# Kernel tuning notes

Measured on AMD Instinct MI355X. Metric: run time of the kernel, lower is better.

Reference implementation:

```python
import jax, jax.numpy as jnp
import numpy as np

EMBED = 1024
HEADS = 16
HEAD_DIM = EMBED // HEADS


def _rope(t):
    # t: (B, S, H, D) -> rotary embedding applied over last dim (GPT-NeoX rotate-half)
    B, S, H, D = t.shape
    half = D // 2
    inv_freq = 1.0 / (10000.0 ** (jnp.arange(0, half, dtype=jnp.float32) / half))
    freqs = jnp.arange(S, dtype=jnp.float32)[:, None] * inv_freq[None, :]  # (S, half)
    cos = jnp.cos(freqs)[None, :, None, :]
    sin = jnp.sin(freqs)[None, :, None, :]
    t1, t2 = t[..., :half], t[..., half:]
    return jnp.concatenate([t1 * cos - t2 * sin, t2 * cos + t1 * sin], axis=-1)


def setup_inputs() -> dict:
    key = jax.random.key(0)
    k1, k2, k3 = jax.random.split(key, 3)
    B, S = 2, 2048
    x = jax.random.normal(k1, (B, S, EMBED), dtype=jnp.float32)
    attn_mask = jnp.ones((B, S), dtype=bool)
    w_qkv = jax.random.normal(k2, (EMBED, 3 * EMBED), dtype=jnp.float32) * (1.0 / np.sqrt(EMBED))
    w_out = jax.random.normal(k3, (EMBED, EMBED), dtype=jnp.float32) * (1.0 / np.sqrt(EMBED))
    return {"x": x, "attn_mask": attn_mask, "w_qkv": w_qkv, "w_out": w_out, "is_causal": 1}


def reference(x, attn_mask, w_qkv, w_out, is_causal):
    B, S, E = x.shape
    qkv = x @ w_qkv                                   # (B, S, 3E)
    q, k, v = jnp.split(qkv, 3, axis=-1)
    q = q.reshape(B, S, HEADS, HEAD_DIM)
    k = k.reshape(B, S, HEADS, HEAD_DIM)
    v = v.reshape(B, S, HEADS, HEAD_DIM)
    q = _rope(q)
    k = _rope(k)
    scale = 1.0 / np.sqrt(HEAD_DIM)
    scores = jnp.einsum('bqhd,bkhd->bhqk', q, k) * scale  # (B, H, S, S)
    neg = jnp.asarray(-1e30, dtype=scores.dtype)
    if is_causal:
        causal = jnp.tril(jnp.ones((S, S), dtype=bool))
        scores = jnp.where(causal[None, None], scores, neg)
    else:
        scores = jnp.where(attn_mask[:, None, None, :], scores, neg)
    attn = jax.nn.softmax(scores, axis=-1)
    y = jnp.einsum('bhqk,bkhd->bqhd', attn, v).reshape(B, S, E)
    return y @ w_out
```

## Files before the change

### kernel.cpp

```cpp
#include <hip/hip_runtime.h>
#include <hip/hip_bf16.h>
#include <stdint.h>

typedef float v4f __attribute__((ext_vector_type(4)));
typedef short v8s __attribute__((ext_vector_type(8)));

#define LOG2E 1.44269504088896f
#define QSCALE (0.125f * LOG2E)
#define SOFTMAX_OFF 16.0f

__device__ __forceinline__ unsigned short f2bf(float f) {
    unsigned int u = __float_as_uint(f);
    u += 0x7fffu + ((u >> 16) & 1u);
    return (unsigned short)(u >> 16);
}

#define LDS_FENCE() __builtin_amdgcn_fence(__ATOMIC_ACQ_REL, "workgroup")

__device__ __forceinline__ void gload_lds16(const unsigned short* g, unsigned short* s) {
    __builtin_amdgcn_global_load_lds(
        (const __attribute__((address_space(1))) unsigned int*)g,
        (__attribute__((address_space(3))) unsigned int*)s, 16, 0, 0);
}

#define BAR()      asm volatile("s_barrier" ::: "memory")
#define VMWAIT(N)  asm volatile("s_waitcnt vmcnt(" #N ")" ::: "memory")
#define LGKM0()    do { asm volatile("s_waitcnt lgkmcnt(0)" ::: "memory"); \
                        __builtin_amdgcn_sched_barrier(0); } while (0)

#define PIPE_BARRIER_KEEP4()                                   \
    do {                                                       \
        asm volatile("s_waitcnt vmcnt(4)" ::: "memory");       \
        __builtin_amdgcn_s_barrier();                          \
        asm volatile("" ::: "memory");                         \
    } while (0)
#define PIPE_BARRIER_DRAIN()                                   \
    do {                                                       \
        asm volatile("s_waitcnt vmcnt(0)" ::: "memory");       \
        __builtin_amdgcn_s_barrier();                          \
        asm volatile("" ::: "memory");                         \
    } while (0)

__global__ void k_prep(const float* __restrict__ x,
                       const float* __restrict__ w_qkv,
                       const float* __restrict__ w_out,
                       unsigned short* __restrict__ xb,
                       unsigned short* __restrict__ wqkvT,
                       unsigned short* __restrict__ woutT,
                       float2* __restrict__ rope) {
    __shared__ unsigned short tile[64][65];
    int id = blockIdx.x, t = threadIdx.x;
    if (id < 1024) {
        int base = id * 256 + t;
#pragma unroll
        for (int k = 0; k < 4; ++k) {
            int i = base + k * 262144;
            float4 v = ((const float4*)x)[i];
            ushort4 o;
            o.x = f2bf(v.x); o.y = f2bf(v.y); o.z = f2bf(v.z); o.w = f2bf(v.w);
            ((ushort4*)xb)[i] = o;
        }
        return;
    }
    id -= 1024;
    if (id < 256) {
        int idx = id * 256 + t;
        int s = idx >> 5, d = idx & 31;
        float inv = __expf(-(float)d * 0.28782313662425572f);
        float sn, cs;
        sincosf((float)s * inv, &sn, &cs);
        rope[idx] = make_float2(cs, sn);
        return;
    }
    id -= 256;
    const float* src; unsigned short* dst; int N, kb, nb;
    if (id < 768) { src = w_qkv; dst = wqkvT; N = 3072; nb = (id % 48) * 64; kb = (id / 48) * 64; }
    else { id -= 768; src = w_out; dst = woutT; N = 1024; nb = (id % 16) * 64; kb = (id / 16) * 64; }
    const int K = 1024;
    for (int i = 0; i < 16; ++i) {
        int e = t + i * 256;
        int n_l = e & 63, k_l = e >> 6;
        tile[n_l][k_l] = f2bf(src[(size_t)(kb + k_l) * N + nb + n_l]);
    }
    __syncthreads();
    for (int i = 0; i < 16; ++i) {
        int e = t + i * 256;
        int k_l = e & 63, n_l = e >> 6;
        dst[(size_t)(nb + n_l) * K + kb + k_l] = tile[n_l][k_l];
    }
}

__global__ __launch_bounds__(512, 2) void k_gemm_qkv(
    const unsigned short* __restrict__ A,
    const unsigned short* __restrict__ Bt,
    const float2* __restrict__ rope,
    unsigned short* __restrict__ Qg,
    unsigned short* __restrict__ Kg,
    unsigned short* __restrict__ Vt) {
    const int K = 1024;
    __shared__ __align__(16) union {
        struct { unsigned short Ab[2][256 * 64], Bb[2][256 * 64]; } g;
        unsigned short vt[4][64][264];
    } sm;
    const int t = threadIdx.x;
    const int w = t >> 6, l = t & 63, quad = l >> 4, ln = l & 15;
    const int wr = w >> 2, wc = w & 3;
    const int mb = blockIdx.y * 256, nb = blockIdx.x * 256;
    const int lxr = l >> 3;
    const int swz = ((l & 7) ^ lxr) * 8;

    v4f acc[8][4];
#pragma unroll
    for (int i = 0; i < 8; ++i)
#pragma unroll
        for (int j = 0; j < 4; ++j) acc[i][j] = (v4f){0.f, 0.f, 0.f, 0.f};

    auto stageHT = [&](const unsigned short* src, int grow, int k0, unsigned short* lds) {
#pragma unroll
        for (int c = 0; c < 2; ++c) {
            int r0 = w * 16 + c * 8;
            gload_lds16(src + (size_t)(grow + r0 + lxr) * K + k0 + swz, lds + r0 * 64);
        }
    };
    auto frag = [&](const unsigned short* base, int row, int g16) -> v8s {
        return *(const v8s*)&base[row * 64 + ((g16 ^ (row & 7)) << 3)];
    };

    v8s aF[4][2], bF0[2][2], bF1[2][2];
    auto readA = [&](const unsigned short* Ap, int ih) {
#pragma unroll
        for (int ii = 0; ii < 4; ++ii) {
            int row = wr * 128 + (ih * 4 + ii) * 16 + ln;
#pragma unroll
            for (int kh = 0; kh < 2; ++kh) aF[ii][kh] = frag(Ap, row, kh * 4 + quad);
        }
    };
    auto readB = [&](const unsigned short* Bp, int jh, v8s (&bF)[2][2]) {
#pragma unroll
        for (int jj = 0; jj < 2; ++jj) {
            int row = wc * 64 + (jh * 2 + jj) * 16 + ln;
#pragma unroll
            for (int kh = 0; kh < 2; ++kh) bF[jj][kh] = frag(Bp, row, kh * 4 + quad);
        }
    };
    auto mfma16 = [&](v8s (&bF)[2][2], int ih, int jh) {
        __builtin_amdgcn_s_setprio(1);
#pragma unroll
        for (int ii = 0; ii < 4; ++ii)
#pragma unroll
            for (int jj = 0; jj < 2; ++jj) {
                v4f* ac = &acc[ih * 4 + ii][jh * 2 + jj];
                *ac = __builtin_amdgcn_mfma_f32_16x16x32_bf16(aF[ii][0], bF[jj][0], *ac, 0, 0, 0);
                *ac = __builtin_amdgcn_mfma_f32_16x16x32_bf16(aF[ii][1], bF[jj][1], *ac, 0, 0, 0);
            }
        __builtin_amdgcn_s_setprio(0);
        __builtin_amdgcn_sched_barrier(0);
    };

    const unsigned short* Ap0 = &sm.g.Ab[0][0];
    const unsigned short* Ap1 = &sm.g.Ab[1][0];
    const unsigned short* Bp0 = &sm.g.Bb[0][0];
    const unsigned short* Bp1 = &sm.g.Bb[1][0];

    stageHT(A,  mb,       0,  &sm.g.Ab[0][0]);
    stageHT(A,  mb + 128, 0,  &sm.g.Ab[0][128 * 64]);
    stageHT(Bt, nb,       0,  &sm.g.Bb[0][0]);
    stageHT(Bt, nb + 128, 0,  &sm.g.Bb[0][128 * 64]);
    stageHT(Bt, nb,       64, &sm.g.Bb[1][0]);
    stageHT(Bt, nb + 128, 64, &sm.g.Bb[1][128 * 64]);
    VMWAIT(4);
    BAR();

    for (int it = 0; it < 8; ++it) {
        const int c1k = (2 * it + 1) * 64, n0k = (2 * it + 2) * 64, n1k = (2 * it + 3) * 64;
        const bool pre = it < 7;
        readA(Ap0, 0); readB(Bp0, 0, bF0);
        stageHT(A, mb, c1k, &sm.g.Ab[1][0]);
        BAR(); LGKM0();
        mfma16(bF0, 0, 0);
        BAR();
        readB(Bp0, 1, bF1);
        stageHT(A, mb + 128, c1k, &sm.g.Ab[1][128 * 64]);
        BAR(); LGKM0();
        mfma16(bF1, 0, 1);
        BAR();
        readA(Ap0, 1);
        if (pre) stageHT(Bt, nb, n0k, &sm.g.Bb[0][0]);
        BAR(); LGKM0();
        mfma16(bF0, 1, 0);
        BAR();
        if (pre) stageHT(Bt, nb + 128, n0k, &sm.g.Bb[0][128 * 64]);
        BAR();
        mfma16(bF1, 1, 1);
        if (pre) VMWAIT(4); else VMWAIT(0);
        BAR();
        readA(Ap1, 0); readB(Bp1, 0, bF0);
        if (pre) stageHT(A, mb, n0k, &sm.g.Ab[0][0]);
        BAR(); LGKM0();
        mfma16(bF0, 0, 0);
        BAR();
        readB(Bp1, 1, bF1);
        if (pre) stageHT(A, mb + 128, n0k, &sm.g.Ab[0][128 * 64]);
        BAR(); LGKM0();
        mfma16(bF1, 0, 1);
        BAR();
        readA(Ap1, 1);
        if (pre) stageHT(Bt, nb, n1k, &sm.g.Bb[1][0]);
        BAR(); LGKM0();
        mfma16(bF0, 1, 0);
        BAR();
        if (pre) stageHT(Bt, nb + 128, n1k, &sm.g.Bb[1][128 * 64]);
        BAR();
        mfma16(bF1, 1, 1);
        if (pre) VMWAIT(4);
        BAR();
    }

    if (nb >= 2048) {
        __syncthreads();
#pragma unroll
        for (int i = 0; i < 8; ++i)
#pragma unroll
            for (int j = 0; j < 4; ++j) {
                int d = j * 16 + ln;
                int s0 = wr * 128 + i * 16 + quad * 4;
                ushort4 pk;
                pk.x = f2bf(acc[i][j][0]); pk.y = f2bf(acc[i][j][1]);
                pk.z = f2bf(acc[i][j][2]); pk.w = f2bf(acc[i][j][3]);
                *(ushort4*)&sm.vt[wc][d][s0] = pk;
            }
        __syncthreads();
        const int hbase = (nb & 1023) >> 6;
        const int b = mb >> 11, sbase = mb & 2047;
#pragma unroll
        for (int i = 0; i < 16; ++i) {
            int c = t + i * 512;
            int h2 = c >> 11, dd = (c >> 5) & 63, off = (c & 31) * 8;
            v8s val = *(const v8s*)&sm.vt[h2][dd][off];
            *(v8s*)(Vt + ((size_t)((b * 16 + hbase + h2) * 64 + dd) * 2048 + sbase + off)) = val;
        }
        return;
    }

    const int nbw = nb + wc * 64;
    const int region = nbw >> 10;
    const int h = (nbw & 1023) >> 6;
    unsigned short* dst = region == 0 ? Qg : Kg;
    const float scale = region == 0 ? QSCALE : 1.0f;
#pragma unroll
    for (int jj = 0; jj < 2; ++jj) {
        const float2* rp = rope + jj * 16 + ln;
#pragma unroll
        for (int i = 0; i < 8; ++i)
#pragma unroll
            for (int r = 0; r < 4; ++r) {
                int row = mb + wr * 128 + i * 16 + quad * 4 + r;
                int s = row & 2047, b = row >> 11;
                float2 cs = rp[s * 32];
                float t1 = acc[i][jj][r], t2 = acc[i][jj + 2][r];
                size_t base = ((size_t)(b * 16 + h) * 2048 + s) * 64;
                dst[base + jj * 16 + ln]      = f2bf((t1 * cs.x - t2 * cs.y) * scale);
                dst[base + jj * 16 + ln + 32] = f2bf((t2 * cs.x + t1 * cs.y) * scale);
            }
    }
}

__global__ __launch_bounds__(256) void k_gemm_out(
    const unsigned short* __restrict__ A,
    const unsigned short* __restrict__ Bt,
    float* __restrict__ C) {
    const int K = 1024, N = 1024;
    __shared__ __align__(16) unsigned short Ab[3][4096];
    __shared__ __align__(16) unsigned short Bb[3][4096];
    const int t = threadIdx.x;
    const int w = t >> 6, l = t & 63, quad = l >> 4, ln = l & 15;
    const int wm = (w >> 1) * 64, wn = (w & 1) * 64;
    const int mb = blockIdx.y * 128, nb = blockIdx.x * 128;

    v4f acc[4][4];
#pragma unroll
    for (int i = 0; i < 4; ++i)
#pragma unroll
        for (int j = 0; j < 4; ++j) acc[i][j] = (v4f){0.f, 0.f, 0.f, 0.f};

    auto stage = [&](int buf, int k0) {
#pragma unroll
        for (int u = 0; u < 2; ++u) {
            int e = t + u * 256;
            gload_lds16(A + (size_t)(mb + (e >> 2)) * K + k0 + (e & 3) * 8,
                        &Ab[buf][(w * 64 + u * 256) * 8]);
            gload_lds16(Bt + (size_t)(nb + (e >> 2)) * K + k0 + (e & 3) * 8,
                        &Bb[buf][(w * 64 + u * 256) * 8]);
        }
    };

    stage(0, 0);
    stage(1, 32);
    int cur = 0, nxt = 2;
    for (int itk = 0; itk < 32; ++itk) {
        if (itk < 31) PIPE_BARRIER_KEEP4();
        else          PIPE_BARRIER_DRAIN();
        if (itk + 2 < 32) {
            stage(nxt, (itk + 2) * 32);
            nxt = nxt == 2 ? 0 : nxt + 1;
        }
        v8s af[4], bfr[4];
#pragma unroll
        for (int i = 0; i < 4; ++i)
            af[i] = *(const v8s*)&Ab[cur][(wm + i * 16 + ln) * 32 + quad * 8];
#pragma unroll
        for (int j = 0; j < 4; ++j)
            bfr[j] = *(const v8s*)&Bb[cur][(wn + j * 16 + ln) * 32 + quad * 8];
#pragma unroll
        for (int i = 0; i < 4; ++i)
#pragma unroll
            for (int j = 0; j < 4; ++j)
                acc[i][j] = __builtin_amdgcn_mfma_f32_16x16x32_bf16(
                    af[i], bfr[j], acc[i][j], 0, 0, 0);
        cur = cur == 2 ? 0 : cur + 1;
    }

#pragma unroll
    for (int i = 0; i < 4; ++i) {
        int r0 = mb + wm + i * 16 + quad * 4;
#pragma unroll
        for (int j = 0; j < 4; ++j) {
            int c0 = nb + wn + j * 16 + ln;
#pragma unroll
            for (int r = 0; r < 4; ++r)
                C[(size_t)(r0 + r) * N + c0] = acc[i][j][r];
        }
    }
}

__global__ __launch_bounds__(256) void k_flash(
    const unsigned short* __restrict__ Qg,
    const unsigned short* __restrict__ Kg,
    const unsigned short* __restrict__ Vt,
    unsigned short* __restrict__ Og) {
    __shared__ __align__(16) unsigned short Kb[2][64 * 64];
    __shared__ __align__(16) unsigned short Vb[2][64 * 64];
    __shared__ __align__(16) unsigned short P[4][16][72];

    const int id = blockIdx.x;
    const int xcd = id & 7, slot = id >> 3;
    const int bh = xcd * 4 + (slot & 3);
    const int qt = 31 - (slot >> 2);
    const int qbase = qt * 64;
    const int nit = qt + 1;

    const int t = threadIdx.x, w = t >> 6, l = t & 63, quad = l >> 4, ln = l & 15;
    const int b = bh >> 4, h = bh & 15;

    const unsigned short* Qp = Qg + (size_t)bh * 2048 * 64;
    const unsigned short* Kp = Kg + (size_t)bh * 2048 * 64;
    const unsigned short* Vp = Vt + (size_t)bh * 64 * 2048;

    unsigned kst[2], vst[2];
    int cchunk = l & 7, rloc = l >> 3;
#pragma unroll
    for (int j = 0; j < 2; ++j) {
        int c = w + j * 4;
        int rr = c * 8 + rloc;
        int g = (cchunk + rr) & 7;
        kst[j] = (unsigned)(rr * 64 + g * 8);
        vst[j] = (unsigned)(rr * 2048 + g * 8);
    }
    const int c0 = ((quad - ln) & 7) * 8;
    const int c1 = ((quad + 4 - ln) & 7) * 8;
    const v8s ones = {0x3F80, 0x3F80, 0x3F80, 0x3F80, 0x3F80, 0x3F80, 0x3F80, 0x3F80};

    const int qrow = qbase + w * 16 + ln;
    v8s qf0 = *(const v8s*)(Qp + (size_t)qrow * 64 + quad * 8);
    v8s qf1 = *(const v8s*)(Qp + (size_t)qrow * 64 + quad * 8 + 32);

    v4f oacc[5];
#pragma unroll
    for (int dt = 0; dt < 5; ++dt) oacc[dt] = (v4f){0.f, 0.f, 0.f, 0.f};

    auto stage = [&](int buf, int kvb) {
        const unsigned short* kg = Kp + (size_t)kvb * 64;
        const unsigned short* vg = Vp + kvb;
#pragma unroll
        for (int j = 0; j < 2; ++j) {
            int c = w + j * 4;
            gload_lds16(kg + kst[j], &Kb[buf][c * 512]);
            gload_lds16(vg + vst[j], &Vb[buf][c * 512]);
        }
    };

    auto compute = [&](int buf, int it) {
        v4f sc[4];
#pragma unroll
        for (int kt = 0; kt < 4; ++kt) {
            int row = kt * 16 + ln;
            v8s k0 = *(const v8s*)&Kb[buf][row * 64 + c0];
            v8s k1 = *(const v8s*)&Kb[buf][row * 64 + c1];
            sc[kt] = (v4f){0.f, 0.f, 0.f, 0.f};
            sc[kt] = __builtin_amdgcn_mfma_f32_16x16x32_bf16(qf0, k0, sc[kt], 0, 0, 0);
            sc[kt] = __builtin_amdgcn_mfma_f32_16x16x32_bf16(qf1, k1, sc[kt], 0, 0, 0);
        }
        if (it == qt) {
            int q0 = qbase + w * 16 + quad * 4;
#pragma unroll
            for (int kt = 0; kt < 4; ++kt) {
                int kv = qbase + kt * 16 + ln;
#pragma unroll
                for (int r = 0; r < 4; ++r)
                    if (kv > q0 + r) sc[kt][r] = -1e30f;
            }
        }
#pragma unroll
        for (int kt = 0; kt < 4; ++kt)
#pragma unroll
            for (int r = 0; r < 4; ++r)
                sc[kt][r] = exp2f(sc[kt][r] - SOFTMAX_OFF);

#pragma unroll
        for (int kt = 0; kt < 4; ++kt) {
            union { __hip_bfloat162 hh; unsigned int u; } p01, p23;
            p01.hh = __float22bfloat162_rn(make_float2(sc[kt][0], sc[kt][1]));
            p23.hh = __float22bfloat162_rn(make_float2(sc[kt][2], sc[kt][3]));
            P[w][quad * 4 + 0][kt * 16 + ln] = (unsigned short)p01.u;
            P[w][quad * 4 + 1][kt * 16 + ln] = (unsigned short)(p01.u >> 16);
            P[w][quad * 4 + 2][kt * 16 + ln] = (unsigned short)p23.u;
            P[w][quad * 4 + 3][kt * 16 + ln] = (unsigned short)(p23.u >> 16);
        }
        LDS_FENCE();
        v8s pf0 = *(const v8s*)&P[w][ln][quad * 8];
        v8s pf1 = *(const v8s*)&P[w][ln][quad * 8 + 32];
        LDS_FENCE();
        __builtin_amdgcn_s_setprio(1);
#pragma unroll
        for (int dt = 0; dt < 4; ++dt) {
            int row = dt * 16 + ln;
            v8s v0 = *(const v8s*)&Vb[buf][row * 64 + c0];
            v8s v1 = *(const v8s*)&Vb[buf][row * 64 + c1];
            oacc[dt] = __builtin_amdgcn_mfma_f32_16x16x32_bf16(pf0, v0, oacc[dt], 0, 0, 0);
            oacc[dt] = __builtin_amdgcn_mfma_f32_16x16x32_bf16(pf1, v1, oacc[dt], 0, 0, 0);
        }
        oacc[4] = __builtin_amdgcn_mfma_f32_16x16x32_bf16(pf0, ones, oacc[4], 0, 0, 0);
        oacc[4] = __builtin_amdgcn_mfma_f32_16x16x32_bf16(pf1, ones, oacc[4], 0, 0, 0);
        __builtin_amdgcn_s_setprio(0);
    };

    stage(0, 0);
    for (int it = 0;;) {
        const int buf = it & 1;
        stage(buf ^ 1, (it + 1) * 64);
        VMWAIT(4);
        BAR();
        compute(buf, it);
        if (++it >= nit) break;
        BAR();
    }

    float rden[4];
#pragma unroll
    for (int r = 0; r < 4; ++r) rden[r] = 1.f / oacc[4][r];
#pragma unroll
    for (int dt = 0; dt < 4; ++dt)
#pragma unroll
        for (int r = 0; r < 4; ++r) {
            int s = qbase + w * 16 + quad * 4 + r;
            Og[(size_t)(b * 2048 + s) * 1024 + h * 64 + dt * 16 + ln] =
                f2bf(oacc[dt][r] * rden[r]);
        }
}

extern "C" void kernel_launch(void* const* d_in, const int* in_sizes, int n_in,
                              void* d_out, int out_size, void* d_ws, size_t ws_size,
                              hipStream_t stream) {
    const float* x     = (const float*)d_in[0];
    const float* w_qkv = (const float*)d_in[2];
    const float* w_out = (const float*)d_in[3];
    char* ws = (char*)d_ws;

    unsigned short* xb    = (unsigned short*)(ws);
    unsigned short* wqkvT = (unsigned short*)(ws + (size_t)(8 << 20));
    unsigned short* woutT = (unsigned short*)(ws + (size_t)(14 << 20));
    unsigned short* Qg    = (unsigned short*)(ws + (size_t)(16 << 20));
    unsigned short* Kg    = (unsigned short*)(ws + (size_t)(24 << 20));
    unsigned short* Vt    = (unsigned short*)(ws + (size_t)(32 << 20));
    unsigned short* Og    = (unsigned short*)(ws + (size_t)(40 << 20));
    float2*         rope  = (float2*)(ws + (size_t)(48 << 20));

    k_prep<<<2304, 256, 0, stream>>>(x, w_qkv, w_out, xb, wqkvT, woutT, rope);
    k_gemm_qkv<<<dim3(12, 16), 512, 0, stream>>>(xb, wqkvT, rope, Qg, Kg, Vt);
    k_flash<<<1024, 256, 0, stream>>>(Qg, Kg, Vt, Og);
    k_gemm_out<<<dim3(8, 32), 256, 0, stream>>>(Og, woutT, (float*)d_out);
}
```

Baseline: 199.0 us.

## Pair causal query tiles per flash block and vectorize QK epilogue stores via LDS

The flash attention kernel now processes two query tiles per block, a short one and its complementary long one, so every block does a balanced amount of causal work and reuses each staged K/V tile for both query tiles. The grid is halved accordingly. The QKV GEMM epilogue writes rotated Q/K values into a padded per-wave LDS buffer and then emits 16-byte coalesced global stores instead of scattered 2-byte stores. Costs are higher register pressure from two accumulator sets and a larger shared-memory union.

```diff
diff --git a/kernel.cpp b/kernel.cpp
--- a/kernel.cpp
+++ b/kernel.cpp
@@ -101,6 +101,7 @@
     __shared__ __align__(16) union {
         struct { unsigned short Ab[2][256 * 64], Bb[2][256 * 64]; } g;
         unsigned short vt[4][64][264];
+        unsigned short qk[8][128][66];
     } sm;
     const int t = threadIdx.x;
     const int w = t >> 6, l = t & 63, quad = l >> 4, ln = l & 15;
@@ -247,6 +248,7 @@
     const int h = (nbw & 1023) >> 6;
     unsigned short* dst = region == 0 ? Qg : Kg;
     const float scale = region == 0 ? QSCALE : 1.0f;
+    unsigned short* qkw = &sm.qk[w][0][0];
 #pragma unroll
     for (int jj = 0; jj < 2; ++jj) {
         const float2* rp = rope + jj * 16 + ln;
@@ -254,14 +256,24 @@
         for (int i = 0; i < 8; ++i)
 #pragma unroll
             for (int r = 0; r < 4; ++r) {
-                int row = mb + wr * 128 + i * 16 + quad * 4 + r;
-                int s = row & 2047, b = row >> 11;
+                int lr = i * 16 + quad * 4 + r;
+                int s = (mb + wr * 128 + lr) & 2047;
                 float2 cs = rp[s * 32];
                 float t1 = acc[i][jj][r], t2 = acc[i][jj + 2][r];
-                size_t base = ((size_t)(b * 16 + h) * 2048 + s) * 64;
-                dst[base + jj * 16 + ln]      = f2bf((t1 * cs.x - t2 * cs.y) * scale);
-                dst[base + jj * 16 + ln + 32] = f2bf((t2 * cs.x + t1 * cs.y) * scale);
+                qkw[lr * 66 + jj * 16 + ln]      = f2bf((t1 * cs.x - t2 * cs.y) * scale);
+                qkw[lr * 66 + jj * 16 + ln + 32] = f2bf((t2 * cs.x + t1 * cs.y) * scale);
             }
+    }
+    LDS_FENCE();
+    const int row0 = mb + wr * 128;
+    const int bb = row0 >> 11, s0 = row0 & 2047;
+    unsigned short* gbase = dst + ((size_t)(bb * 16 + h) * 2048 + s0) * 64;
+#pragma unroll
+    for (int itn = 0; itn < 16; ++itn) {
+        int c = itn * 64 + l;
+        int lr = c >> 3, off = (c & 7) * 8;
+        v8s val = *(const v8s*)&qkw[lr * 66 + off];
+        *(v8s*)(gbase + (size_t)lr * 64 + off) = val;
     }
 }
 
@@ -345,9 +357,9 @@
     const int id = blockIdx.x;
     const int xcd = id & 7, slot = id >> 3;
     const int bh = xcd * 4 + (slot & 3);
-    const int qt = 31 - (slot >> 2);
-    const int qbase = qt * 64;
-    const int nit = qt + 1;
+    const int pair = slot >> 2;
+    const int qtA = pair;
+    const int qtB = 31 - pair;
 
     const int t = threadIdx.x, w = t >> 6, l = t & 63, quad = l >> 4, ln = l & 15;
     const int b = bh >> 4, h = bh & 15;
@@ -370,13 +382,19 @@
     const int c1 = ((quad + 4 - ln) & 7) * 8;
     const v8s ones = {0x3F80, 0x3F80, 0x3F80, 0x3F80, 0x3F80, 0x3F80, 0x3F80, 0x3F80};
 
-    const int qrow = qbase + w * 16 + ln;
-    v8s qf0 = *(const v8s*)(Qp + (size_t)qrow * 64 + quad * 8);
-    v8s qf1 = *(const v8s*)(Qp + (size_t)qrow * 64 + quad * 8 + 32);
-
-    v4f oacc[5];
-#pragma unroll
-    for (int dt = 0; dt < 5; ++dt) oacc[dt] = (v4f){0.f, 0.f, 0.f, 0.f};
+    const int qrA = qtA * 64 + w * 16 + ln;
+    const int qrB = qtB * 64 + w * 16 + ln;
+    v8s qfA0 = *(const v8s*)(Qp + (size_t)qrA * 64 + quad * 8);
+    v8s qfA1 = *(const v8s*)(Qp + (size_t)qrA * 64 + quad * 8 + 32);
+    v8s qfB0 = *(const v8s*)(Qp + (size_t)qrB * 64 + quad * 8);
+    v8s qfB1 = *(const v8s*)(Qp + (size_t)qrB * 64 + quad * 8 + 32);
+
+    v4f oaccA[5], oaccB[5];
+#pragma unroll
+    for (int dt = 0; dt < 5; ++dt) {
+        oaccA[dt] = (v4f){0.f, 0.f, 0.f, 0.f};
+        oaccB[dt] = (v4f){0.f, 0.f, 0.f, 0.f};
+    }
 
     auto stage = [&](int buf, int kvb) {
         const unsigned short* kg = Kp + (size_t)kvb * 64;
@@ -389,7 +407,7 @@
         }
     };
 
-    auto compute = [&](int buf, int it) {
+    auto computeT = [&](int buf, int it, int qt, v8s qf0, v8s qf1, v4f* oacc) {
         v4f sc[4];
 #pragma unroll
         for (int kt = 0; kt < 4; ++kt) {
@@ -401,10 +419,10 @@
             sc[kt] = __builtin_amdgcn_mfma_f32_16x16x32_bf16(qf1, k1, sc[kt], 0, 0, 0);
         }
         if (it == qt) {
-            int q0 = qbase + w * 16 + quad * 4;
+            int q0 = qt * 64 + w * 16 + quad * 4;
 #pragma unroll
             for (int kt = 0; kt < 4; ++kt) {
-                int kv = qbase + kt * 16 + ln;
+                int kv = qt * 64 + kt * 16 + ln;
 #pragma unroll
                 for (int r = 0; r < 4; ++r)
                     if (kv > q0 + r) sc[kt][r] = -1e30f;
@@ -447,25 +465,31 @@
     stage(0, 0);
     for (int it = 0;;) {
         const int buf = it & 1;
-        stage(buf ^ 1, (it + 1) * 64);
-        VMWAIT(4);
-        BAR();
-        compute(buf, it);
-        if (++it >= nit) break;
-        BAR();
-    }
-
-    float rden[4];
-#pragma unroll
-    for (int r = 0; r < 4; ++r) rden[r] = 1.f / oacc[4][r];
-#pragma unroll
-    for (int dt = 0; dt < 4; ++dt)
-#pragma unroll
-        for (int r = 0; r < 4; ++r) {
-            int s = qbase + w * 16 + quad * 4 + r;
-            Og[(size_t)(b * 2048 + s) * 1024 + h * 64 + dt * 16 + ln] =
-                f2bf(oacc[dt][r] * rden[r]);
-        }
+        if (it < qtB) { stage(buf ^ 1, (it + 1) * 64); VMWAIT(4); }
+        else          { VMWAIT(0); }
+        BAR();
+        if (it <= qtA) computeT(buf, it, qtA, qfA0, qfA1, oaccA);
+        computeT(buf, it, qtB, qfB0, qfB1, oaccB);
+        if (++it > qtB) break;
+        BAR();
+    }
+
+#pragma unroll
+    for (int tile = 0; tile < 2; ++tile) {
+        const v4f* oacc = tile == 0 ? oaccA : oaccB;
+        const int qbase = (tile == 0 ? qtA : qtB) * 64;
+        float rden[4];
+#pragma unroll
+        for (int r = 0; r < 4; ++r) rden[r] = 1.f / oacc[4][r];
+#pragma unroll
+        for (int dt = 0; dt < 4; ++dt)
+#pragma unroll
+            for (int r = 0; r < 4; ++r) {
+                int s = qbase + w * 16 + quad * 4 + r;
+                Og[(size_t)(b * 2048 + s) * 1024 + h * 64 + dt * 16 + ln] =
+                    f2bf(oacc[dt][r] * rden[r]);
+            }
+    }
 }
 
 extern "C" void kernel_launch(void* const* d_in, const int* in_sizes, int n_in,
@@ -487,6 +511,6 @@
 
     k_prep<<<2304, 256, 0, stream>>>(x, w_qkv, w_out, xb, wqkvT, woutT, rope);
     k_gemm_qkv<<<dim3(12, 16), 512, 0, stream>>>(xb, wqkvT, rope, Qg, Kg, Vt);
-    k_flash<<<1024, 256, 0, stream>>>(Qg, Kg, Vt, Og);
+    k_flash<<<512, 256, 0, stream>>>(Qg, Kg, Vt, Og);
     k_gemm_out<<<dim3(8, 32), 256, 0, stream>>>(Og, woutT, (float*)d_out);
 }
```

New measurement: 193.6 us. -2.7%, faster.

## Stage QKV epilogue through LDS and reuse K buffer for P in flash

Applied to the files above, without the earlier changes.

The QKV GEMM epilogue now writes the rotary-embedded Q/K values into a padded per-wave LDS tile and then copies them to global memory with coalesced 16-byte stores, replacing scattered 2-byte global stores. The flash kernel drops its separate P buffer and writes the probabilities into the already-consumed K buffer with an XOR swizzle, adding a barrier first so other waves are done with K. Together with a launch bound of 4 blocks per CU, this is meant to cut LDS use and raise occupancy. The extra barrier per iteration may add stalls, and the K buffer reuse needs careful ordering against the next stage's prefetch.

```diff
diff --git a/kernel.cpp b/kernel.cpp
--- a/kernel.cpp
+++ b/kernel.cpp
@@ -101,6 +101,7 @@
     __shared__ __align__(16) union {
         struct { unsigned short Ab[2][256 * 64], Bb[2][256 * 64]; } g;
         unsigned short vt[4][64][264];
+        unsigned short qk[8][128][66];
     } sm;
     const int t = threadIdx.x;
     const int w = t >> 6, l = t & 63, quad = l >> 4, ln = l & 15;
@@ -247,6 +248,7 @@
     const int h = (nbw & 1023) >> 6;
     unsigned short* dst = region == 0 ? Qg : Kg;
     const float scale = region == 0 ? QSCALE : 1.0f;
+    unsigned short* qkw = &sm.qk[w][0][0];
 #pragma unroll
     for (int jj = 0; jj < 2; ++jj) {
         const float2* rp = rope + jj * 16 + ln;
@@ -254,14 +256,24 @@
         for (int i = 0; i < 8; ++i)
 #pragma unroll
             for (int r = 0; r < 4; ++r) {
-                int row = mb + wr * 128 + i * 16 + quad * 4 + r;
-                int s = row & 2047, b = row >> 11;
+                int lr = i * 16 + quad * 4 + r;
+                int s = (mb + wr * 128 + lr) & 2047;
                 float2 cs = rp[s * 32];
                 float t1 = acc[i][jj][r], t2 = acc[i][jj + 2][r];
-                size_t base = ((size_t)(b * 16 + h) * 2048 + s) * 64;
-                dst[base + jj * 16 + ln]      = f2bf((t1 * cs.x - t2 * cs.y) * scale);
-                dst[base + jj * 16 + ln + 32] = f2bf((t2 * cs.x + t1 * cs.y) * scale);
+                qkw[lr * 66 + jj * 16 + ln]      = f2bf((t1 * cs.x - t2 * cs.y) * scale);
+                qkw[lr * 66 + jj * 16 + ln + 32] = f2bf((t2 * cs.x + t1 * cs.y) * scale);
             }
+    }
+    LDS_FENCE();
+    const int row0 = mb + wr * 128;
+    const int bb = row0 >> 11, s0 = row0 & 2047;
+    unsigned short* gbase = dst + ((size_t)(bb * 16 + h) * 2048 + s0) * 64;
+#pragma unroll
+    for (int itn = 0; itn < 16; ++itn) {
+        int c = itn * 64 + l;
+        int lr = c >> 3, off = (c & 7) * 8;
+        v8s val = *(const v8s*)&qkw[lr * 66 + off];
+        *(v8s*)(gbase + (size_t)lr * 64 + off) = val;
     }
 }
 
@@ -333,14 +345,13 @@
     }
 }
 
-__global__ __launch_bounds__(256) void k_flash(
+__global__ __launch_bounds__(256, 4) void k_flash(
     const unsigned short* __restrict__ Qg,
     const unsigned short* __restrict__ Kg,
     const unsigned short* __restrict__ Vt,
     unsigned short* __restrict__ Og) {
     __shared__ __align__(16) unsigned short Kb[2][64 * 64];
     __shared__ __align__(16) unsigned short Vb[2][64 * 64];
-    __shared__ __align__(16) unsigned short P[4][16][72];
 
     const int id = blockIdx.x;
     const int xcd = id & 7, slot = id >> 3;
@@ -416,19 +427,24 @@
             for (int r = 0; r < 4; ++r)
                 sc[kt][r] = exp2f(sc[kt][r] - SOFTMAX_OFF);
 
+        BAR();
+        unsigned short* Pw = &Kb[buf][w * 1024];
+        const int gcol = ln & 7;
 #pragma unroll
         for (int kt = 0; kt < 4; ++kt) {
             union { __hip_bfloat162 hh; unsigned int u; } p01, p23;
             p01.hh = __float22bfloat162_rn(make_float2(sc[kt][0], sc[kt][1]));
             p23.hh = __float22bfloat162_rn(make_float2(sc[kt][2], sc[kt][3]));
-            P[w][quad * 4 + 0][kt * 16 + ln] = (unsigned short)p01.u;
-            P[w][quad * 4 + 1][kt * 16 + ln] = (unsigned short)(p01.u >> 16);
-            P[w][quad * 4 + 2][kt * 16 + ln] = (unsigned short)p23.u;
-            P[w][quad * 4 + 3][kt * 16 + ln] = (unsigned short)(p23.u >> 16);
+            int gq = kt * 2 + (ln >> 3);
+            int r0w = quad * 4;
+            Pw[(r0w + 0) * 64 + ((gq ^ ((r0w + 0) & 7)) << 3) + gcol] = (unsigned short)p01.u;
+            Pw[(r0w + 1) * 64 + ((gq ^ ((r0w + 1) & 7)) << 3) + gcol] = (unsigned short)(p01.u >> 16);
+            Pw[(r0w + 2) * 64 + ((gq ^ ((r0w + 2) & 7)) << 3) + gcol] = (unsigned short)p23.u;
+            Pw[(r0w + 3) * 64 + ((gq ^ ((r0w + 3) & 7)) << 3) + gcol] = (unsigned short)(p23.u >> 16);
         }
         LDS_FENCE();
-        v8s pf0 = *(const v8s*)&P[w][ln][quad * 8];
-        v8s pf1 = *(const v8s*)&P[w][ln][quad * 8 + 32];
+        v8s pf0 = *(const v8s*)&Pw[ln * 64 + ((quad ^ (ln & 7)) << 3)];
+        v8s pf1 = *(const v8s*)&Pw[ln * 64 + (((quad + 4) ^ (ln & 7)) << 3)];
         LDS_FENCE();
         __builtin_amdgcn_s_setprio(1);
 #pragma unroll
```

Result: faster. 190.3 us (-4.4%).
